# Optimization experiments

Measured on AMD Instinct MI355X. Metric: run time of the kernel, lower is better.

Reference implementation:

```python
import jax, jax.numpy as jnp
import numpy as np

N, E, B = 50000, 800000, 512
DIN, H, G, M = 128, 128, 32, 128
EPS = 1e-5


def _gcn_layer(h, src, dst, W, b):
    h = h @ W  # [N, H]
    loop = jnp.arange(N)
    s = jnp.concatenate([src, loop])
    d = jnp.concatenate([dst, loop])
    deg = jax.ops.segment_sum(jnp.ones(s.shape, h.dtype), d, num_segments=N)
    dinv = jax.lax.rsqrt(jnp.maximum(deg, 1.0))  # deg >= 1 due to self-loops
    norm = dinv[s] * dinv[d]  # [E+N]
    out = jax.ops.segment_sum(norm[:, None] * h[s], d, num_segments=N)
    return out + b


def _bn_relu(h, gamma, beta):
    mu = jnp.mean(h, axis=0)
    var = jnp.mean((h - mu) ** 2, axis=0)
    return jax.nn.relu((h - mu) * jax.lax.rsqrt(var + EPS) * gamma + beta)


def setup_inputs() -> dict:
    key = jax.random.key(0)
    ks = jax.random.split(key, 20)
    inp = {
        "x": jax.random.normal(ks[0], (N, DIN), jnp.float32),
        "edge_index": jax.random.randint(ks[1], (2, E), 0, N),
        "batch": jnp.sort(jax.random.randint(ks[2], (N,), 0, B)),
        "global_feats": jax.random.normal(ks[3], (B, G), jnp.float32),
    }
    dims = [DIN, H, H]
    for i in range(3):
        inp[f"W{i}"] = jax.random.normal(ks[4 + i], (dims[i], H), jnp.float32) / np.sqrt(dims[i])
        inp[f"b{i}"] = jnp.zeros((H,), jnp.float32)
        inp[f"g{i}"] = jnp.ones((H,), jnp.float32)
        inp[f"be{i}"] = jnp.zeros((H,), jnp.float32)
    inp["M1w"] = jax.random.normal(ks[10], (H + G, M), jnp.float32) / np.sqrt(H + G)
    inp["M1b"] = jnp.zeros((M,), jnp.float32)
    inp["M2w"] = jax.random.normal(ks[11], (M, M // 2), jnp.float32) / np.sqrt(M)
    inp["M2b"] = jnp.zeros((M // 2,), jnp.float32)
    inp["M3w"] = jax.random.normal(ks[12], (M // 2, 1), jnp.float32) / np.sqrt(M // 2)
    inp["M3b"] = jnp.zeros((1,), jnp.float32)
    return inp


def reference(x, edge_index, batch, global_feats,
              W0, b0, g0, be0, W1, b1, g1, be1, W2, b2, g2, be2,
              M1w, M1b, M2w, M2b, M3w, M3b):
    src, dst = edge_index[0], edge_index[1]
    h = x
    for W, b, g, be in ((W0, b0, g0, be0), (W1, b1, g1, be1), (W2, b2, g2, be2)):
        h = _bn_relu(_gcn_layer(h, src, dst, W, b), g, be)
    # global mean pool over graphs
    sums = jax.ops.segment_sum(h, batch, num_segments=B)  # [B, H]
    cnt = jax.ops.segment_sum(jnp.ones((N,), h.dtype), batch, num_segments=B)
    pooled = sums / jnp.maximum(cnt, 1.0)[:, None]
    z = jnp.concatenate([pooled, global_feats], axis=1)  # [B, H+G]
    z = jax.nn.relu(z @ M1w + M1b)
    z = jax.nn.relu(z @ M2w + M2b)
    out = z @ M3w + M3b  # [B, 1]
    return out.reshape(-1)
```

## Files before the change

kernel.cpp:

```cpp
#include <hip/hip_runtime.h>

#define NN 50000
#define NE 800000
#define BG 512
#define HD 128
#define GD 32
#define MD 128
#define EPSV 1e-5f
#define NBK 256
#define BSTR 196
#define BCAP 4096
#define SP 136
#define CSB 512

typedef __attribute__((ext_vector_type(8))) short bf16x8;
typedef __attribute__((ext_vector_type(4))) float f32x4;

static __device__ __forceinline__ unsigned short f2bf(float f) {
    unsigned int u = __float_as_uint(f);
    u += 0x7fffu + ((u >> 16) & 1u);
    return (unsigned short)(u >> 16);
}
static __device__ __forceinline__ float bf_lo(unsigned int v) {
    return __uint_as_float(v << 16);
}
static __device__ __forceinline__ float bf_hi(unsigned int v) {
    return __uint_as_float(v & 0xffff0000u);
}

__global__ __launch_bounds__(256) void k_bin(const int* __restrict__ src,
                                             const int* __restrict__ dst,
                                             int* __restrict__ bucket_cnt,
                                             unsigned int* __restrict__ binned) {
    __shared__ int hcnt[NBK];
    __shared__ int hbase[NBK];
    int tid = threadIdx.x;
    int e0 = blockIdx.x * 2048;
    unsigned int pv[8];
    int bk[8], rk[8];
#pragma unroll
    for (int i = 0; i < 8; ++i) {
        int e = e0 + i * 256 + tid;
        if (e < NE) {
            int s = src[e];
            int d = dst[e];
            bk[i] = d / BSTR;
            pv[i] = ((unsigned int)(d - bk[i] * BSTR) << 16) | (unsigned int)s;
        } else {
            bk[i] = -1;
        }
    }
    hcnt[tid] = 0;
    __syncthreads();
#pragma unroll
    for (int i = 0; i < 8; ++i)
        if (bk[i] >= 0) rk[i] = atomicAdd(&hcnt[bk[i]], 1);
    __syncthreads();
    hbase[tid] = atomicAdd(&bucket_cnt[tid], hcnt[tid]);
    __syncthreads();
#pragma unroll
    for (int i = 0; i < 8; ++i)
        if (bk[i] >= 0)
            binned[(size_t)bk[i] * BCAP + hbase[bk[i]] + rk[i]] = pv[i];
}

__global__ __launch_bounds__(256) void k_bscan(const int* __restrict__ bucket_cnt,
                                               int* __restrict__ bpre) {
    __shared__ int ls[NBK];
    int t = threadIdx.x;
    int v = bucket_cnt[t];
    ls[t] = v;
    __syncthreads();
    for (int off = 1; off < NBK; off <<= 1) {
        int cur = ls[t];
        int add = (t >= off) ? ls[t - off] : 0;
        __syncthreads();
        ls[t] = cur + add;
        __syncthreads();
    }
    bpre[t] = ls[t] - v;
}

__global__ __launch_bounds__(256) void k_cnt2(const unsigned int* __restrict__ binned,
                                              const int* __restrict__ bucket_cnt,
                                              const int* __restrict__ bpre,
                                              int* __restrict__ offsets,
                                              float* __restrict__ dinv) {
    __shared__ int h[BSTR];
    __shared__ int ls[256];
    int b = blockIdx.x, t = threadIdx.x;
    if (t < BSTR) h[t] = 0;
    __syncthreads();
    int nb = bucket_cnt[b];
    const unsigned int* base = binned + (size_t)b * BCAP;
    for (int e = t; e < nb; e += 256)
        atomicAdd(&h[base[e] >> 16], 1);
    __syncthreads();
    int c = (t < BSTR) ? h[t] : 0;
    ls[t] = c;
    __syncthreads();
    for (int off = 1; off < 256; off <<= 1) {
        int cur = ls[t];
        int add = (t >= off) ? ls[t - off] : 0;
        __syncthreads();
        ls[t] = cur + add;
        __syncthreads();
    }
    int node = b * BSTR + t;
    if (t < BSTR && node < NN) {
        offsets[node] = ls[t] - c + bpre[b];
        dinv[node] = rsqrtf((float)(c + 1));
        if (node == NN - 1) offsets[NN] = NE;
    }
}

__global__ __launch_bounds__(256) void k_fill2(const unsigned int* __restrict__ binned,
                                               const int* __restrict__ bucket_cnt,
                                               const int* __restrict__ offsets,
                                               int* __restrict__ csr) {
    __shared__ int cur[BSTR];
    int b = blockIdx.x, t = threadIdx.x;
    int node = b * BSTR + t;
    if (t < BSTR) cur[t] = (node < NN) ? offsets[node] : 0;
    __syncthreads();
    int nb = bucket_cnt[b];
    const unsigned int* base = binned + (size_t)b * BCAP;
    for (int e = t; e < nb; e += 256) {
        unsigned int v = base[e];
        int pos = atomicAdd(&cur[v >> 16], 1);
        csr[pos] = (int)(v & 0xffffu);
    }
}

__global__ __launch_bounds__(256) void k_wtrans(const float* __restrict__ W0,
                                                const float* __restrict__ W1,
                                                const float* __restrict__ W2,
                                                unsigned short* __restrict__ Wt) {
    __shared__ unsigned short sW[128 * 130];
    const float* Wsrc = blockIdx.x == 0 ? W0 : (blockIdx.x == 1 ? W1 : W2);
#pragma unroll
    for (int i = 0; i < 64; ++i) {
        int idx = i * 256 + threadIdx.x;
        int k = idx >> 7, n = idx & 127;
        sW[n * 130 + k] = f2bf(Wsrc[idx]);
    }
    __syncthreads();
    unsigned short* o = Wt + (size_t)blockIdx.x * 16384;
#pragma unroll
    for (int i = 0; i < 64; ++i) {
        int idx = i * 256 + threadIdx.x;
        int n = idx >> 7, k = idx & 127;
        o[idx] = sW[n * 130 + k];
    }
}

__global__ __launch_bounds__(256) void k_gemm(const float* __restrict__ In,
                                              const unsigned short* __restrict__ Wt,
                                              unsigned short* __restrict__ Th,
                                              const float* __restrict__ ss,
                                              const float* __restrict__ dinv,
                                              int useBN) {
    __shared__ unsigned short Abf[64 * SP];
    __shared__ unsigned short WtL[128 * SP];
    int tid = threadIdx.x;
    int rowBase = blockIdx.x * 64;
#pragma unroll
    for (int i = 0; i < 8; ++i) {
        int q = tid + i * 256;
        int row = q >> 5;
        int c4 = (q & 31) * 4;
        int rg = rowBase + row;
        if (rg >= NN) rg = NN - 1;
        float4 v = *(const float4*)&In[(size_t)rg * HD + c4];
        if (useBN) {
            float4 sc = *(const float4*)&ss[c4];
            float4 sh = *(const float4*)&ss[128 + c4];
            v.x = fmaxf(v.x * sc.x + sh.x, 0.f);
            v.y = fmaxf(v.y * sc.y + sh.y, 0.f);
            v.z = fmaxf(v.z * sc.z + sh.z, 0.f);
            v.w = fmaxf(v.w * sc.w + sh.w, 0.f);
        }
        unsigned short* p = &Abf[row * SP + c4];
        p[0] = f2bf(v.x); p[1] = f2bf(v.y); p[2] = f2bf(v.z); p[3] = f2bf(v.w);
    }
#pragma unroll
    for (int i = 0; i < 8; ++i) {
        int q = tid + i * 256;
        int n = q >> 4;
        int k8 = (q & 15) * 8;
        bf16x8 w = *(const bf16x8*)&Wt[n * HD + k8];
        *(bf16x8*)&WtL[n * SP + k8] = w;
    }
    __syncthreads();
    int lane = tid & 63;
    int wv = tid >> 6;
    int quad = lane >> 4;
    int lrow = wv * 16 + (lane & 15);
    f32x4 acc[8];
#pragma unroll
    for (int c = 0; c < 8; ++c) acc[c] = (f32x4){0.f, 0.f, 0.f, 0.f};
#pragma unroll
    for (int qk = 0; qk < 4; ++qk) {
        int ko = quad * 8 + qk * 32;
        bf16x8 bfr = *(const bf16x8*)&Abf[lrow * SP + ko];
#pragma unroll
        for (int c = 0; c < 8; ++c) {
            bf16x8 afr = *(const bf16x8*)&WtL[(c * 16 + (lane & 15)) * SP + ko];
            acc[c] = __builtin_amdgcn_mfma_f32_16x16x32_bf16(afr, bfr, acc[c], 0, 0, 0);
        }
    }
    int grow = rowBase + lrow;
    if (grow < NN) {
        float di = dinv[grow];
#pragma unroll
        for (int c = 0; c < 8; ++c) {
            ushort4 o;
            o.x = f2bf(acc[c][0] * di);
            o.y = f2bf(acc[c][1] * di);
            o.z = f2bf(acc[c][2] * di);
            o.w = f2bf(acc[c][3] * di);
            *(ushort4*)&Th[(size_t)grow * HD + c * 16 + quad * 4] = o;
        }
    }
}

__global__ __launch_bounds__(256, 8) void k_aggregate(const uint2* __restrict__ T2,
                                                      const int* __restrict__ offsets,
                                                      const int* __restrict__ csr,
                                                      const float* __restrict__ dinv,
                                                      const float* __restrict__ bias,
                                                      float* __restrict__ A) {
    int d = blockIdx.x * 4 + (threadIdx.x >> 6);
    int l = threadIdx.x & 63;
    int half = l >> 5;
    int li = l & 31;
    if (d >= NN) return;
    int start = offsets[d], end = offsets[d + 1];
    float a0 = 0.f, a1 = 0.f, a2 = 0.f, a3 = 0.f;
    int j = start;
    for (; j + 15 < end; j += 16) {
        int s[8];
        uint2 v[8];
#pragma unroll
        for (int i = 0; i < 8; ++i) s[i] = csr[j + 2 * i + half];
#pragma unroll
        for (int i = 0; i < 8; ++i) v[i] = T2[(size_t)s[i] * 32 + li];
#pragma unroll
        for (int i = 0; i < 8; ++i) {
            a0 += bf_lo(v[i].x); a1 += bf_hi(v[i].x);
            a2 += bf_lo(v[i].y); a3 += bf_hi(v[i].y);
        }
    }
    for (; j + 7 < end; j += 8) {
        int s0 = csr[j + half];
        int s1 = csr[j + 2 + half];
        int s2 = csr[j + 4 + half];
        int s3 = csr[j + 6 + half];
        uint2 v0 = T2[(size_t)s0 * 32 + li];
        uint2 v1 = T2[(size_t)s1 * 32 + li];
        uint2 v2 = T2[(size_t)s2 * 32 + li];
        uint2 v3 = T2[(size_t)s3 * 32 + li];
        a0 += bf_lo(v0.x); a1 += bf_hi(v0.x); a2 += bf_lo(v0.y); a3 += bf_hi(v0.y);
        a0 += bf_lo(v1.x); a1 += bf_hi(v1.x); a2 += bf_lo(v1.y); a3 += bf_hi(v1.y);
        a0 += bf_lo(v2.x); a1 += bf_hi(v2.x); a2 += bf_lo(v2.y); a3 += bf_hi(v2.y);
        a0 += bf_lo(v3.x); a1 += bf_hi(v3.x); a2 += bf_lo(v3.y); a3 += bf_hi(v3.y);
    }
    for (; j + 1 < end; j += 2) {
        int s0 = csr[j + half];
        uint2 v0 = T2[(size_t)s0 * 32 + li];
        a0 += bf_lo(v0.x); a1 += bf_hi(v0.x); a2 += bf_lo(v0.y); a3 += bf_hi(v0.y);
    }
    if (j < end && half == 0) {
        int s0 = csr[j];
        uint2 v0 = T2[(size_t)s0 * 32 + li];
        a0 += bf_lo(v0.x); a1 += bf_hi(v0.x); a2 += bf_lo(v0.y); a3 += bf_hi(v0.y);
    }
    a0 += __shfl_xor(a0, 32);
    a1 += __shfl_xor(a1, 32);
    a2 += __shfl_xor(a2, 32);
    a3 += __shfl_xor(a3, 32);
    if (half == 0) {
        float di = dinv[d];
        uint2 vd = T2[(size_t)d * 32 + li];
        float4 bs = *(const float4*)&bias[4 * li];
        float4 o;
        o.x = di * (a0 + bf_lo(vd.x)) + bs.x;
        o.y = di * (a1 + bf_hi(vd.x)) + bs.y;
        o.z = di * (a2 + bf_lo(vd.y)) + bs.z;
        o.w = di * (a3 + bf_hi(vd.y)) + bs.w;
        *(float4*)&A[(size_t)d * HD + 4 * li] = o;
    }
}

__global__ __launch_bounds__(256) void k_colstats(const float4* __restrict__ A4,
                                                  float* __restrict__ pstats) {
    int li = threadIdx.x & 31;
    int rr = threadIdx.x >> 5;
    float4 s = {0.f, 0.f, 0.f, 0.f}, q = {0.f, 0.f, 0.f, 0.f};
    for (int row = blockIdx.x * 8 + rr; row < NN; row += gridDim.x * 8) {
        float4 v = A4[(size_t)row * 32 + li];
        s.x += v.x; s.y += v.y; s.z += v.z; s.w += v.w;
        q.x += v.x * v.x; q.y += v.y * v.y; q.z += v.z * v.z; q.w += v.w * v.w;
    }
    __shared__ float4 lsum[256], lqum[256];
    lsum[threadIdx.x] = s;
    lqum[threadIdx.x] = q;
    __syncthreads();
    if (rr == 0) {
        float4 a = lsum[li];
#pragma unroll
        for (int g = 1; g < 8; ++g) {
            float4 b = lsum[g * 32 + li];
            a.x += b.x; a.y += b.y; a.z += b.z; a.w += b.w;
        }
        *(float4*)&pstats[blockIdx.x * 256 + 4 * li] = a;
    } else if (rr == 1) {
        float4 a = lqum[li];
#pragma unroll
        for (int g = 1; g < 8; ++g) {
            float4 b = lqum[g * 32 + li];
            a.x += b.x; a.y += b.y; a.z += b.z; a.w += b.w;
        }
        *(float4*)&pstats[blockIdx.x * 256 + 128 + 4 * li] = a;
    }
}

__global__ __launch_bounds__(256) void k_bnfinal(const float* __restrict__ pstats,
                                                 const float* __restrict__ gamma,
                                                 const float* __restrict__ beta,
                                                 float* __restrict__ ss) {
    __shared__ float sums[256];
    int t = threadIdx.x;
    float a = 0.f;
    for (int b = 0; b < CSB; ++b) a += pstats[b * 256 + t];
    sums[t] = a;
    __syncthreads();
    if (t < 128) {
        float mu = sums[t] * (1.f / NN);
        float var = sums[128 + t] * (1.f / NN) - mu * mu;
        float sc = gamma[t] * rsqrtf(var + EPSV);
        ss[t] = sc;
        ss[128 + t] = beta[t] - mu * sc;
    }
}

__global__ __launch_bounds__(256) void k_pool(const float* __restrict__ A,
                                              const int* __restrict__ batch,
                                              const float* __restrict__ ss,
                                              float* __restrict__ pooled) {
    int t = threadIdx.x;
    int f = t & 127, half = t >> 7;
    int r0 = blockIdx.x * 64;
    int rend = min(r0 + 64, NN);
    float s = ss[f], h = ss[128 + f];
    float acc = 0.f;
    int cg = -1;
    for (int r = r0 + half; r < rend; r += 2) {
        int g = batch[r];
        if (g != cg) {
            if (cg >= 0) atomicAdd(&pooled[(size_t)cg * HD + f], acc);
            cg = g;
            acc = 0.f;
        }
        acc += fmaxf(A[(size_t)r * HD + f] * s + h, 0.f);
    }
    if (cg >= 0) atomicAdd(&pooled[(size_t)cg * HD + f], acc);
}

__global__ __launch_bounds__(128) void k_mlp(const float* __restrict__ pooled,
                                             const int* __restrict__ batch,
                                             const float* __restrict__ gfeat,
                                             const float* __restrict__ M1w,
                                             const float* __restrict__ M1b,
                                             const float* __restrict__ M2w,
                                             const float* __restrict__ M2b,
                                             const float* __restrict__ M3w,
                                             const float* __restrict__ M3b,
                                             float* __restrict__ out) {
    __shared__ int sb[2];
    __shared__ float z[HD + GD];
    __shared__ float z1[MD];
    __shared__ float z2[MD / 2];
    int b = blockIdx.x, t = threadIdx.x;
    if (t < 2) {
        int val = b + t;
        int lo = 0, hi = NN;
        while (lo < hi) {
            int mid = (lo + hi) >> 1;
            if (batch[mid] < val) lo = mid + 1; else hi = mid;
        }
        sb[t] = lo;
    }
    __syncthreads();
    float ic = 1.f / fmaxf((float)(sb[1] - sb[0]), 1.f);
    z[t] = pooled[(size_t)b * HD + t] * ic;
    if (t < GD) z[HD + t] = gfeat[b * GD + t];
    __syncthreads();
    float a = M1b[t];
    for (int k = 0; k < HD + GD; ++k) a += z[k] * M1w[k * MD + t];
    z1[t] = fmaxf(a, 0.f);
    __syncthreads();
    if (t < MD / 2) {
        float a2 = M2b[t];
        for (int k = 0; k < MD; ++k) a2 += z1[k] * M2w[k * (MD / 2) + t];
        z2[t] = fmaxf(a2, 0.f);
    }
    __syncthreads();
    if (t < 64) {
        float p = z2[t] * M3w[t];
#pragma unroll
        for (int off = 32; off; off >>= 1) p += __shfl_down(p, off);
        if (t == 0) out[b] = p + M3b[0];
    }
}

static inline size_t alg(size_t x) { return (x + 255) & ~(size_t)255; }

extern "C" void kernel_launch(void* const* d_in, const int* in_sizes, int n_in,
                              void* d_out, int out_size, void* d_ws, size_t ws_size,
                              hipStream_t stream) {
    const float* x = (const float*)d_in[0];
    const int* ei = (const int*)d_in[1];
    const int* batch = (const int*)d_in[2];
    const float* gf = (const float*)d_in[3];
    const float* W[3] = {(const float*)d_in[4], (const float*)d_in[8], (const float*)d_in[12]};
    const float* bb[3] = {(const float*)d_in[5], (const float*)d_in[9], (const float*)d_in[13]};
    const float* gg[3] = {(const float*)d_in[6], (const float*)d_in[10], (const float*)d_in[14]};
    const float* be[3] = {(const float*)d_in[7], (const float*)d_in[11], (const float*)d_in[15]};
    const float* M1w = (const float*)d_in[16];
    const float* M1b = (const float*)d_in[17];
    const float* M2w = (const float*)d_in[18];
    const float* M2b = (const float*)d_in[19];
    const float* M3w = (const float*)d_in[20];
    const float* M3b = (const float*)d_in[21];
    float* out = (float*)d_out;

    char* w = (char*)d_ws;
    int* bucket_cnt = (int*)w;    w += alg((size_t)NBK * 4);
    int* bpre = (int*)w;          w += alg((size_t)NBK * 4);
    int* offsets = (int*)w;       w += alg((size_t)(NN + 1) * 4);
    int* csr = (int*)w;           w += alg((size_t)NE * 4);
    float* dinv = (float*)w;      w += alg((size_t)NN * 4);
    float* pstats = (float*)w;    w += alg((size_t)CSB * 256 * 4);
    float* ss = (float*)w;        w += alg(256 * 4);
    float* pooled = (float*)w;    w += alg((size_t)BG * HD * 4);
    unsigned short* Wt = (unsigned short*)w;  w += alg((size_t)3 * 16384 * 2);
    unsigned int* binned = (unsigned int*)w;  w += alg((size_t)NBK * BCAP * 4);
    float* A = (float*)w;         w += alg((size_t)NN * HD * 4);
    unsigned short* Th = (unsigned short*)w;  w += alg((size_t)NN * HD * 2);

    const int* src = ei;
    const int* dst = ei + NE;

    hipMemsetAsync(bucket_cnt, 0, (size_t)NBK * 4, stream);
    k_bin<<<(NE + 2047) / 2048, 256, 0, stream>>>(src, dst, bucket_cnt, binned);
    k_bscan<<<1, 256, 0, stream>>>(bucket_cnt, bpre);
    k_cnt2<<<NBK, 256, 0, stream>>>(binned, bucket_cnt, bpre, offsets, dinv);
    k_fill2<<<NBK, 256, 0, stream>>>(binned, bucket_cnt, offsets, csr);
    k_wtrans<<<3, 256, 0, stream>>>(W[0], W[1], W[2], Wt);

    const float* hin = x;
    for (int L = 0; L < 3; ++L) {
        k_gemm<<<(NN + 63) / 64, 256, 0, stream>>>(hin, Wt + (size_t)L * 16384, Th, ss,
                                                   dinv, L > 0);
        k_aggregate<<<(NN + 3) / 4, 256, 0, stream>>>((const uint2*)Th, offsets, csr,
                                                      dinv, bb[L], A);
        k_colstats<<<CSB, 256, 0, stream>>>((const float4*)A, pstats);
        k_bnfinal<<<1, 256, 0, stream>>>(pstats, gg[L], be[L], ss);
        hin = A;
    }

    hipMemsetAsync(pooled, 0, (size_t)BG * HD * 4, stream);
    k_pool<<<(NN + 63) / 64, 256, 0, stream>>>(A, batch, ss, pooled);
    k_mlp<<<BG, 128, 0, stream>>>(pooled, batch, gf, M1w, M1b, M2w, M2b, M3w, M3b, out);
}
```

Measured before the change: 379.8 us.

## Store layer activations in bf16 and fuse CSR build and BN-finalize kernels

```diff
diff --git a/kernel.cpp b/kernel.cpp
--- a/kernel.cpp
+++ b/kernel.cpp
@@ -21,6 +21,9 @@
     u += 0x7fffu + ((u >> 16) & 1u);
     return (unsigned short)(u >> 16);
 }
+static __device__ __forceinline__ float bfu(unsigned short v) {
+    return __uint_as_float((unsigned int)v << 16);
+}
 static __device__ __forceinline__ float bf_lo(unsigned int v) {
     return __uint_as_float(v << 16);
 }
@@ -64,33 +67,30 @@
             binned[(size_t)bk[i] * BCAP + hbase[bk[i]] + rk[i]] = pv[i];
 }
 
-__global__ __launch_bounds__(256) void k_bscan(const int* __restrict__ bucket_cnt,
-                                               int* __restrict__ bpre) {
-    __shared__ int ls[NBK];
-    int t = threadIdx.x;
-    int v = bucket_cnt[t];
-    ls[t] = v;
-    __syncthreads();
-    for (int off = 1; off < NBK; off <<= 1) {
-        int cur = ls[t];
+__global__ __launch_bounds__(256) void k_csr(const unsigned int* __restrict__ binned,
+                                             const int* __restrict__ bucket_cnt,
+                                             int* __restrict__ offsets,
+                                             float* __restrict__ dinv,
+                                             int* __restrict__ csr) {
+    __shared__ int ls[256];
+    __shared__ int h[BSTR];
+    __shared__ int cur[BSTR];
+    __shared__ int bpre_s;
+    int b = blockIdx.x, t = threadIdx.x;
+    int bc = bucket_cnt[t];
+    ls[t] = bc;
+    __syncthreads();
+    for (int off = 1; off < 256; off <<= 1) {
+        int c0 = ls[t];
         int add = (t >= off) ? ls[t - off] : 0;
         __syncthreads();
-        ls[t] = cur + add;
+        ls[t] = c0 + add;
         __syncthreads();
     }
-    bpre[t] = ls[t] - v;
-}
-
-__global__ __launch_bounds__(256) void k_cnt2(const unsigned int* __restrict__ binned,
-                                              const int* __restrict__ bucket_cnt,
-                                              const int* __restrict__ bpre,
-                                              int* __restrict__ offsets,
-                                              float* __restrict__ dinv) {
-    __shared__ int h[BSTR];
-    __shared__ int ls[256];
-    int b = blockIdx.x, t = threadIdx.x;
+    if (t == b) bpre_s = ls[t] - bc;
     if (t < BSTR) h[t] = 0;
     __syncthreads();
+    int bpre = bpre_s;
     int nb = bucket_cnt[b];
     const unsigned int* base = binned + (size_t)b * BCAP;
     for (int e = t; e < nb; e += 256)
@@ -100,31 +100,23 @@
     ls[t] = c;
     __syncthreads();
     for (int off = 1; off < 256; off <<= 1) {
-        int cur = ls[t];
+        int c0 = ls[t];
         int add = (t >= off) ? ls[t - off] : 0;
         __syncthreads();
-        ls[t] = cur + add;
+        ls[t] = c0 + add;
         __syncthreads();
     }
     int node = b * BSTR + t;
-    if (t < BSTR && node < NN) {
-        offsets[node] = ls[t] - c + bpre[b];
-        dinv[node] = rsqrtf((float)(c + 1));
-        if (node == NN - 1) offsets[NN] = NE;
-    }
-}
-
-__global__ __launch_bounds__(256) void k_fill2(const unsigned int* __restrict__ binned,
-                                               const int* __restrict__ bucket_cnt,
-                                               const int* __restrict__ offsets,
-                                               int* __restrict__ csr) {
-    __shared__ int cur[BSTR];
-    int b = blockIdx.x, t = threadIdx.x;
-    int node = b * BSTR + t;
-    if (t < BSTR) cur[t] = (node < NN) ? offsets[node] : 0;
-    __syncthreads();
-    int nb = bucket_cnt[b];
-    const unsigned int* base = binned + (size_t)b * BCAP;
+    if (t < BSTR) {
+        int excl = ls[t] - c + bpre;
+        cur[t] = excl;
+        if (node < NN) {
+            offsets[node] = excl;
+            dinv[node] = rsqrtf((float)(c + 1));
+            if (node == NN - 1) offsets[NN] = NE;
+        }
+    }
+    __syncthreads();
     for (int e = t; e < nb; e += 256) {
         unsigned int v = base[e];
         int pos = atomicAdd(&cur[v >> 16], 1);
@@ -154,7 +146,8 @@
     }
 }
 
-__global__ __launch_bounds__(256) void k_gemm(const float* __restrict__ In,
+__global__ __launch_bounds__(256) void k_gemm(const float* __restrict__ Inf,
+                                              const unsigned short* __restrict__ Inh,
                                               const unsigned short* __restrict__ Wt,
                                               unsigned short* __restrict__ Th,
                                               const float* __restrict__ ss,
@@ -164,24 +157,36 @@
     __shared__ unsigned short WtL[128 * SP];
     int tid = threadIdx.x;
     int rowBase = blockIdx.x * 64;
-#pragma unroll
-    for (int i = 0; i < 8; ++i) {
-        int q = tid + i * 256;
-        int row = q >> 5;
-        int c4 = (q & 31) * 4;
-        int rg = rowBase + row;
-        if (rg >= NN) rg = NN - 1;
-        float4 v = *(const float4*)&In[(size_t)rg * HD + c4];
-        if (useBN) {
-            float4 sc = *(const float4*)&ss[c4];
-            float4 sh = *(const float4*)&ss[128 + c4];
-            v.x = fmaxf(v.x * sc.x + sh.x, 0.f);
-            v.y = fmaxf(v.y * sc.y + sh.y, 0.f);
-            v.z = fmaxf(v.z * sc.z + sh.z, 0.f);
-            v.w = fmaxf(v.w * sc.w + sh.w, 0.f);
-        }
-        unsigned short* p = &Abf[row * SP + c4];
-        p[0] = f2bf(v.x); p[1] = f2bf(v.y); p[2] = f2bf(v.z); p[3] = f2bf(v.w);
+    if (useBN) {
+#pragma unroll
+        for (int i = 0; i < 4; ++i) {
+            int q = tid + i * 256;
+            int row = q >> 4;
+            int k8 = (q & 15) * 8;
+            int rg = rowBase + row;
+            if (rg >= NN) rg = NN - 1;
+            bf16x8 raw = *(const bf16x8*)&Inh[(size_t)rg * HD + k8];
+            unsigned short o[8];
+#pragma unroll
+            for (int e = 0; e < 8; ++e) {
+                float v = bfu((unsigned short)raw[e]);
+                v = fmaxf(v * ss[k8 + e] + ss[128 + k8 + e], 0.f);
+                o[e] = f2bf(v);
+            }
+            *(bf16x8*)&Abf[row * SP + k8] = *(bf16x8*)o;
+        }
+    } else {
+#pragma unroll
+        for (int i = 0; i < 8; ++i) {
+            int q = tid + i * 256;
+            int row = q >> 5;
+            int c4 = (q & 31) * 4;
+            int rg = rowBase + row;
+            if (rg >= NN) rg = NN - 1;
+            float4 v = *(const float4*)&Inf[(size_t)rg * HD + c4];
+            unsigned short* p = &Abf[row * SP + c4];
+            p[0] = f2bf(v.x); p[1] = f2bf(v.y); p[2] = f2bf(v.z); p[3] = f2bf(v.w);
+        }
     }
 #pragma unroll
     for (int i = 0; i < 8; ++i) {
@@ -229,7 +234,7 @@
                                                       const int* __restrict__ csr,
                                                       const float* __restrict__ dinv,
                                                       const float* __restrict__ bias,
-                                                      float* __restrict__ A) {
+                                                      unsigned short* __restrict__ Ah) {
     int d = blockIdx.x * 4 + (threadIdx.x >> 6);
     int l = threadIdx.x & 63;
     int half = l >> 5;
@@ -283,26 +288,32 @@
         float di = dinv[d];
         uint2 vd = T2[(size_t)d * 32 + li];
         float4 bs = *(const float4*)&bias[4 * li];
-        float4 o;
-        o.x = di * (a0 + bf_lo(vd.x)) + bs.x;
-        o.y = di * (a1 + bf_hi(vd.x)) + bs.y;
-        o.z = di * (a2 + bf_lo(vd.y)) + bs.z;
-        o.w = di * (a3 + bf_hi(vd.y)) + bs.w;
-        *(float4*)&A[(size_t)d * HD + 4 * li] = o;
-    }
-}
-
-__global__ __launch_bounds__(256) void k_colstats(const float4* __restrict__ A4,
-                                                  float* __restrict__ pstats) {
+        ushort4 o;
+        o.x = f2bf(di * (a0 + bf_lo(vd.x)) + bs.x);
+        o.y = f2bf(di * (a1 + bf_hi(vd.x)) + bs.y);
+        o.z = f2bf(di * (a2 + bf_lo(vd.y)) + bs.z);
+        o.w = f2bf(di * (a3 + bf_hi(vd.y)) + bs.w);
+        *(ushort4*)&Ah[(size_t)d * HD + 4 * li] = o;
+    }
+}
+
+__global__ __launch_bounds__(256) void k_colstats(const uint2* __restrict__ A2,
+                                                  float* __restrict__ pstats,
+                                                  int* __restrict__ ctr,
+                                                  const float* __restrict__ gamma,
+                                                  const float* __restrict__ beta,
+                                                  float* __restrict__ ss) {
     int li = threadIdx.x & 31;
     int rr = threadIdx.x >> 5;
     float4 s = {0.f, 0.f, 0.f, 0.f}, q = {0.f, 0.f, 0.f, 0.f};
-    for (int row = blockIdx.x * 8 + rr; row < NN; row += gridDim.x * 8) {
-        float4 v = A4[(size_t)row * 32 + li];
-        s.x += v.x; s.y += v.y; s.z += v.z; s.w += v.w;
-        q.x += v.x * v.x; q.y += v.y * v.y; q.z += v.z * v.z; q.w += v.w * v.w;
+    for (int row = blockIdx.x * 8 + rr; row < NN; row += CSB * 8) {
+        uint2 u = A2[(size_t)row * 32 + li];
+        float x0 = bf_lo(u.x), x1 = bf_hi(u.x), x2 = bf_lo(u.y), x3 = bf_hi(u.y);
+        s.x += x0; s.y += x1; s.z += x2; s.w += x3;
+        q.x += x0 * x0; q.y += x1 * x1; q.z += x2 * x2; q.w += x3 * x3;
     }
     __shared__ float4 lsum[256], lqum[256];
+    __shared__ int isLast;
     lsum[threadIdx.x] = s;
     lqum[threadIdx.x] = q;
     __syncthreads();
@@ -323,48 +334,62 @@
         }
         *(float4*)&pstats[blockIdx.x * 256 + 128 + 4 * li] = a;
     }
-}
-
-__global__ __launch_bounds__(256) void k_bnfinal(const float* __restrict__ pstats,
-                                                 const float* __restrict__ gamma,
-                                                 const float* __restrict__ beta,
-                                                 float* __restrict__ ss) {
-    __shared__ float sums[256];
-    int t = threadIdx.x;
-    float a = 0.f;
-    for (int b = 0; b < CSB; ++b) a += pstats[b * 256 + t];
-    sums[t] = a;
-    __syncthreads();
-    if (t < 128) {
-        float mu = sums[t] * (1.f / NN);
-        float var = sums[128 + t] * (1.f / NN) - mu * mu;
-        float sc = gamma[t] * rsqrtf(var + EPSV);
-        ss[t] = sc;
-        ss[128 + t] = beta[t] - mu * sc;
-    }
-}
-
-__global__ __launch_bounds__(256) void k_pool(const float* __restrict__ A,
+    __threadfence();
+    __syncthreads();
+    if (threadIdx.x == 0) {
+        int old = atomicAdd(ctr, 1);
+        isLast = (old == CSB - 1);
+    }
+    __syncthreads();
+    if (isLast) {
+        __threadfence();
+        int t = threadIdx.x;
+        float a = 0.f;
+        for (int b = 0; b < CSB; ++b) a += pstats[b * 256 + t];
+        __shared__ float sums[256];
+        sums[t] = a;
+        __syncthreads();
+        if (t < 128) {
+            float mu = sums[t] * (1.f / NN);
+            float var = sums[128 + t] * (1.f / NN) - mu * mu;
+            float sc = gamma[t] * rsqrtf(var + EPSV);
+            ss[t] = sc;
+            ss[128 + t] = beta[t] - mu * sc;
+        }
+    }
+}
+
+__global__ __launch_bounds__(256) void k_pool(const unsigned int* __restrict__ Au,
                                               const int* __restrict__ batch,
                                               const float* __restrict__ ss,
                                               float* __restrict__ pooled) {
     int t = threadIdx.x;
-    int f = t & 127, half = t >> 7;
+    int fu = t & 63;
+    int half = t >> 6;
     int r0 = blockIdx.x * 64;
     int rend = min(r0 + 64, NN);
-    float s = ss[f], h = ss[128 + f];
-    float acc = 0.f;
+    float s0 = ss[2 * fu], s1 = ss[2 * fu + 1];
+    float h0 = ss[128 + 2 * fu], h1 = ss[128 + 2 * fu + 1];
+    float a0 = 0.f, a1 = 0.f;
     int cg = -1;
-    for (int r = r0 + half; r < rend; r += 2) {
+    for (int r = r0 + half; r < rend; r += 4) {
         int g = batch[r];
         if (g != cg) {
-            if (cg >= 0) atomicAdd(&pooled[(size_t)cg * HD + f], acc);
+            if (cg >= 0) {
+                atomicAdd(&pooled[(size_t)cg * HD + 2 * fu], a0);
+                atomicAdd(&pooled[(size_t)cg * HD + 2 * fu + 1], a1);
+            }
             cg = g;
-            acc = 0.f;
-        }
-        acc += fmaxf(A[(size_t)r * HD + f] * s + h, 0.f);
-    }
-    if (cg >= 0) atomicAdd(&pooled[(size_t)cg * HD + f], acc);
+            a0 = 0.f; a1 = 0.f;
+        }
+        unsigned int v = Au[(size_t)r * 64 + fu];
+        a0 += fmaxf(bf_lo(v) * s0 + h0, 0.f);
+        a1 += fmaxf(bf_hi(v) * s1 + h1, 0.f);
+    }
+    if (cg >= 0) {
+        atomicAdd(&pooled[(size_t)cg * HD + 2 * fu], a0);
+        atomicAdd(&pooled[(size_t)cg * HD + 2 * fu + 1], a1);
+    }
 }
 
 __global__ __launch_bounds__(128) void k_mlp(const float* __restrict__ pooled,
@@ -437,7 +462,7 @@
 
     char* w = (char*)d_ws;
     int* bucket_cnt = (int*)w;    w += alg((size_t)NBK * 4);
-    int* bpre = (int*)w;          w += alg((size_t)NBK * 4);
+    int* ctr = (int*)w;           w += alg(3 * 4);
     int* offsets = (int*)w;       w += alg((size_t)(NN + 1) * 4);
     int* csr = (int*)w;           w += alg((size_t)NE * 4);
     float* dinv = (float*)w;      w += alg((size_t)NN * 4);
@@ -446,31 +471,27 @@
     float* pooled = (float*)w;    w += alg((size_t)BG * HD * 4);
     unsigned short* Wt = (unsigned short*)w;  w += alg((size_t)3 * 16384 * 2);
     unsigned int* binned = (unsigned int*)w;  w += alg((size_t)NBK * BCAP * 4);
-    float* A = (float*)w;         w += alg((size_t)NN * HD * 4);
+    unsigned short* Ah = (unsigned short*)w;  w += alg((size_t)NN * HD * 2);
     unsigned short* Th = (unsigned short*)w;  w += alg((size_t)NN * HD * 2);
 
     const int* src = ei;
     const int* dst = ei + NE;
 
-    hipMemsetAsync(bucket_cnt, 0, (size_t)NBK * 4, stream);
+    hipMemsetAsync(bucket_cnt, 0, alg((size_t)NBK * 4) + alg(3 * 4), stream);
     k_bin<<<(NE + 2047) / 2048, 256, 0, stream>>>(src, dst, bucket_cnt, binned);
-    k_bscan<<<1, 256, 0, stream>>>(bucket_cnt, bpre);
-    k_cnt2<<<NBK, 256, 0, stream>>>(binned, bucket_cnt, bpre, offsets, dinv);
-    k_fill2<<<NBK, 256, 0, stream>>>(binned, bucket_cnt, offsets, csr);
+    k_csr<<<NBK, 256, 0, stream>>>(binned, bucket_cnt, offsets, dinv, csr);
     k_wtrans<<<3, 256, 0, stream>>>(W[0], W[1], W[2], Wt);
 
-    const float* hin = x;
     for (int L = 0; L < 3; ++L) {
-        k_gemm<<<(NN + 63) / 64, 256, 0, stream>>>(hin, Wt + (size_t)L * 16384, Th, ss,
+        k_gemm<<<(NN + 63) / 64, 256, 0, stream>>>(x, Ah, Wt + (size_t)L * 16384, Th, ss,
                                                    dinv, L > 0);
         k_aggregate<<<(NN + 3) / 4, 256, 0, stream>>>((const uint2*)Th, offsets, csr,
-                                                      dinv, bb[L], A);
-        k_colstats<<<CSB, 256, 0, stream>>>((const float4*)A, pstats);
-        k_bnfinal<<<1, 256, 0, stream>>>(pstats, gg[L], be[L], ss);
-        hin = A;
+                                                      dinv, bb[L], Ah);
+        k_colstats<<<CSB, 256, 0, stream>>>((const uint2*)Ah, pstats, ctr + L,
+                                            gg[L], be[L], ss);
     }
 
     hipMemsetAsync(pooled, 0, (size_t)BG * HD * 4, stream);
-    k_pool<<<(NN + 63) / 64, 256, 0, stream>>>(A, batch, ss, pooled);
+    k_pool<<<(NN + 63) / 64, 256, 0, stream>>>((const unsigned int*)Ah, batch, ss, pooled);
     k_mlp<<<BG, 128, 0, stream>>>(pooled, batch, gf, M1w, M1b, M2w, M2b, M3w, M3b, out);
 }
```

Result: slower. 466.4 us (+22.8%).
